# Performance work log

Measured on AMD Instinct MI355X. Metric: run time of the kernel, lower is better.

The kernel has to match this reference:

```python
import jax, jax.numpy as jnp
import numpy as np

NUM_HEADS = 4
B, C, N = 2, 128, 4096
NS = N // 2


def setup_inputs() -> dict:
    key = jax.random.key(0)
    ks = jax.random.split(key, 10)
    # idx_select/idx_drop together form a permutation of [0, N) per batch
    perms = jax.vmap(lambda k: jax.random.permutation(k, N))(jax.random.split(ks[8], B))
    idx_select = perms[:, :NS][:, None, :].astype(jnp.int64)
    idx_drop = perms[:, NS:][:, None, :].astype(jnp.int64)
    return {
        "pcd_up": jax.random.normal(ks[0], (B, C, N), jnp.float32),
        "points_select": jax.random.normal(ks[1], (B, C, NS), jnp.float32),
        "points_drop": jax.random.normal(ks[2], (B, C, NS), jnp.float32),
        "pcd_up_xyz": jax.random.normal(ks[3], (B, 3, N), jnp.float32),
        "Wq": jax.random.normal(ks[4], (C, C), jnp.float32) * 0.05,
        "Wk": jax.random.normal(ks[5], (C, C), jnp.float32) * 0.05,
        "Wv": jax.random.normal(ks[6], (C, C), jnp.float32) * 0.05,
        "Wskip": jax.random.normal(ks[7], (C, C), jnp.float32) * 0.05,
        "idx_select": idx_select,
        "idx_drop": idx_drop,
    }


def _concat_by_idx(a, b, idx_a, idx_b):
    # torch: target.scatter(-1, idx, cat([a,b],-1)) with idx expanded over channels
    src = jnp.concatenate([a, b], axis=-1)                  # [B, C, N]
    idx = jnp.concatenate([idx_a, idx_b], axis=-1)[:, 0, :]  # [B, N]
    return jax.vmap(lambda s, i: jnp.zeros_like(s).at[:, i].set(s))(src, idx)


def reference(pcd_up, points_select, points_drop, pcd_up_xyz, Wq, Wk, Wv, Wskip,
              idx_select, idx_drop):
    x = _concat_by_idx(points_select, points_drop, idx_select, idx_drop)  # [B,C,N]
    b, _, n = x.shape

    def proj_split(W, xx):
        y = jnp.einsum('oc,bcn->bon', W, xx)  # 1x1 Conv1d, no bias
        return y.reshape(b, NUM_HEADS, y.shape[1] // NUM_HEADS, n)  # [B,H,D,N]

    q = proj_split(Wq, x)
    k = proj_split(Wk, x)
    v = proj_split(Wv, x)
    dq = q.shape[2]
    # energy = q^T @ k, scaled by sqrt(q_depth)
    energy = jnp.einsum('bhdn,bhdm->bhnm', q, k) / jnp.sqrt(jnp.asarray(dq, x.dtype))
    attn = jax.nn.softmax(energy, axis=-1)                   # [B,H,N,N]
    out = jnp.einsum('bhnm,bhdm->bhnd', attn, v)             # [B,H,N,Dv]
    out = out.transpose(0, 2, 1, 3).reshape(b, n, -1).transpose(0, 2, 1)  # [B,v_out,N]
    return out + jnp.einsum('oc,bcn->bon', Wskip, pcd_up)
```

## Files before the change

kernel.cpp:

```cpp
#include <hip/hip_runtime.h>
#include <cstdint>

#define B_ 2
#define C_ 128
#define N_ 4096
#define H_ 4
#define D_ 32

typedef unsigned short ushort_t;
typedef __attribute__((ext_vector_type(8))) short bf16x8;
typedef __attribute__((ext_vector_type(4))) float f32x4;
typedef __attribute__((ext_vector_type(4))) unsigned int u32x4;

__device__ __forceinline__ ushort_t f2bf(float f) {
  unsigned int u = __builtin_bit_cast(unsigned int, f);
  u += 0x7fffu + ((u >> 16) & 1u);
  return (ushort_t)(u >> 16);
}

__device__ __forceinline__ void stage16(const ushort_t* g, ushort_t* l) {
  __builtin_amdgcn_global_load_lds(
      (const __attribute__((address_space(1))) unsigned int*)g,
      (__attribute__((address_space(3))) unsigned int*)l, 16, 0, 0);
}

__global__ __launch_bounds__(256) void k_prep(const float* __restrict__ psel,
                                              const float* __restrict__ pdrop,
                                              const int* __restrict__ isel,
                                              const int* __restrict__ idrop,
                                              const float* __restrict__ Wq,
                                              const float* __restrict__ Wk,
                                              const float* __restrict__ Wv,
                                              const float* __restrict__ Wsk,
                                              ushort_t* __restrict__ xT,
                                              ushort_t* __restrict__ Wb) {
  int z = blockIdx.z;
  int t = threadIdx.x;
  if (z == 2) {
    int idx = blockIdx.y * 64 + blockIdx.x;
    int m = idx >> 5, sub = idx & 31;
    const float* src = (m == 0) ? Wq : (m == 1) ? Wk : (m == 2) ? Wv : Wsk;
    float sc = (m == 0) ? 0.25506552f : 1.0f;
    int e = sub * 512 + t * 2;
    float2 v = *(const float2*)(src + e);
    unsigned int u = ((unsigned int)f2bf(v.y * sc) << 16) | (unsigned int)f2bf(v.x * sc);
    ((unsigned int*)Wb)[m * 8192 + (e >> 1)] = u;
    return;
  }
  const float* src = z ? pdrop : psel;
  const int* idx = z ? idrop : isel;
  __shared__ ushort_t tile[128][34];
  int b = blockIdx.y;
  int i0 = blockIdx.x * 32;
  {
    int c = t >> 1, ih = (t & 1) * 16;
    const float4* p = (const float4*)(src + ((size_t)(b * 128 + c) * 2048 + i0 + ih));
#pragma unroll
    for (int g = 0; g < 4; ++g) {
      float4 v = p[g];
      tile[c][ih + g * 4 + 0] = f2bf(v.x);
      tile[c][ih + g * 4 + 1] = f2bf(v.y);
      tile[c][ih + g * 4 + 2] = f2bf(v.z);
      tile[c][ih + g * 4 + 3] = f2bf(v.w);
    }
  }
  __syncthreads();
  {
    int i = t >> 3, c0 = (t & 7) * 16;
    int n = idx[b * 2048 + i0 + i];
    alignas(16) ushort_t outv[16];
#pragma unroll
    for (int j = 0; j < 16; ++j) outv[j] = tile[c0 + j][i];
    uint4* q = (uint4*)(xT + ((size_t)(b * 4096 + n) * 128 + c0));
    q[0] = *(uint4*)outv; q[1] = *(uint4*)(outv + 8);
  }
}

__global__ __launch_bounds__(256) void k_proj(const ushort_t* __restrict__ xT,
                                              const float* __restrict__ pcd,
                                              const ushort_t* __restrict__ Wb,
                                              ushort_t* __restrict__ Kb,
                                              ushort_t* __restrict__ Vt,
                                              float* __restrict__ outp) {
  __shared__ ushort_t ldsT[64][136];
  __shared__ float y[128][66];
  int n0 = blockIdx.x * 64, wt = blockIdx.y, b = blockIdx.z, t = threadIdx.x;
  int wave = t >> 6, lane = t & 63, lr = lane & 15, quad = lane >> 4;
  const ushort_t* W = Wb + (size_t)(wt + 1) * 16384;

  if (wt == 2) {
#pragma unroll
    for (int rep = 0; rep < 4; ++rep) {
      int idx = rep * 256 + t;
      int c = idx >> 3, ng = (idx & 7) * 8;
      const float4* p = (const float4*)(pcd + ((size_t)(b * 128 + c) * 4096 + n0 + ng));
      float4 v0 = p[0], v1 = p[1];
      ldsT[ng + 0][c] = f2bf(v0.x); ldsT[ng + 1][c] = f2bf(v0.y);
      ldsT[ng + 2][c] = f2bf(v0.z); ldsT[ng + 3][c] = f2bf(v0.w);
      ldsT[ng + 4][c] = f2bf(v1.x); ldsT[ng + 5][c] = f2bf(v1.y);
      ldsT[ng + 6][c] = f2bf(v1.z); ldsT[ng + 7][c] = f2bf(v1.w);
    }
    __syncthreads();
  }

  f32x4 acc[2][4];
#pragma unroll
  for (int mt = 0; mt < 2; ++mt)
#pragma unroll
    for (int nt = 0; nt < 4; ++nt) acc[mt][nt] = (f32x4){0.f, 0.f, 0.f, 0.f};
#pragma unroll
  for (int kc = 0; kc < 128; kc += 32) {
    bf16x8 a[2], bb[4];
#pragma unroll
    for (int mt = 0; mt < 2; ++mt)
      a[mt] = *(const bf16x8*)(W + (size_t)(wave * 32 + mt * 16 + lr) * 128 + kc + quad * 8);
    if (wt == 2) {
#pragma unroll
      for (int nt = 0; nt < 4; ++nt)
        bb[nt] = *(const bf16x8*)(&ldsT[nt * 16 + lr][kc + quad * 8]);
    } else {
#pragma unroll
      for (int nt = 0; nt < 4; ++nt)
        bb[nt] = *(const bf16x8*)(xT + ((size_t)(b * 4096 + n0 + nt * 16 + lr)) * 128 + kc + quad * 8);
    }
#pragma unroll
    for (int mt = 0; mt < 2; ++mt)
#pragma unroll
      for (int nt = 0; nt < 4; ++nt)
        acc[mt][nt] = __builtin_amdgcn_mfma_f32_16x16x32_bf16(a[mt], bb[nt], acc[mt][nt], 0, 0, 0);
  }

  if (wt == 2) {
#pragma unroll
    for (int mt = 0; mt < 2; ++mt)
#pragma unroll
      for (int nt = 0; nt < 4; ++nt)
#pragma unroll
        for (int r = 0; r < 4; ++r) {
          int o = wave * 32 + mt * 16 + quad * 4 + r;
          outp[(size_t)(b * 128 + o) * 4096 + n0 + nt * 16 + lr] = acc[mt][nt][r];
        }
    return;
  }

#pragma unroll
  for (int mt = 0; mt < 2; ++mt)
#pragma unroll
    for (int nt = 0; nt < 4; ++nt)
#pragma unroll
      for (int r = 0; r < 4; ++r)
        y[wave * 32 + mt * 16 + quad * 4 + r][nt * 16 + lr] = acc[mt][nt][r];
  __syncthreads();

  if (wt == 0) {
    int n = t >> 2, dq = (t & 3) * 8;
#pragma unroll
    for (int h = 0; h < 4; ++h) {
      alignas(16) ushort_t vals[8];
#pragma unroll
      for (int j = 0; j < 8; ++j) vals[j] = f2bf(y[h * 32 + dq + j][n]);
      *(uint4*)(Kb + (((size_t)(b * 4 + h) * 4096 + n0 + n) * 32 + dq)) = *(uint4*)vals;
    }
  } else {
    int o = t >> 1, half = t & 1;
    int h = o >> 5, d = o & 31;
    alignas(16) ushort_t vals[32];
#pragma unroll
    for (int j = 0; j < 32; ++j) {
      int c = half * 32 + ((j >> 3) * 4 + (j & 3) + ((j & 4) << 2));
      vals[j] = f2bf(y[o][c]);
    }
    uint4* dst = (uint4*)(Vt + ((size_t)(b * 4 + h) * 32 + d) * 4096 + n0 + half * 32);
#pragma unroll
    for (int g = 0; g < 4; ++g) dst[g] = *(uint4*)(vals + g * 8);
  }
}

__global__ __launch_bounds__(256) void k_attn(const ushort_t* __restrict__ xT,
                                              const ushort_t* __restrict__ Wb,
                                              const ushort_t* __restrict__ Kb,
                                              const ushort_t* __restrict__ Vt,
                                              float* __restrict__ outp) {
  __shared__ ushort_t qT[4][32 * 40];
  __shared__ ushort_t kbuf[2][4096];
  __shared__ ushort_t vbuf[2][4096];
  __shared__ float obuf[4][32 * 33];

  int bh = blockIdx.x & 7;
  int q0 = (blockIdx.x >> 3) * 128;
  int b = bh >> 2, h = bh & 3;
  int t = threadIdx.x, wave = t >> 6, lane = t & 63, lr = lane & 15, quad = lane >> 4;
  int qbase = q0 + wave * 32;
  const ushort_t* xb = xT + (size_t)b * N_ * 128;
  const ushort_t* wqp = Wb + (size_t)h * 32 * 128;
  const ushort_t* Kp = Kb + (size_t)bh * N_ * 32;
  const ushort_t* Vp = Vt + (size_t)bh * 32 * N_;

  {
    f32x4 accq[2][2];
#pragma unroll
    for (int mt = 0; mt < 2; ++mt)
#pragma unroll
      for (int nt = 0; nt < 2; ++nt) accq[mt][nt] = (f32x4){0.f, 0.f, 0.f, 0.f};
#pragma unroll
    for (int kc = 0; kc < 128; kc += 32) {
      bf16x8 ax[2], bw[2];
#pragma unroll
      for (int mt = 0; mt < 2; ++mt)
        ax[mt] = *(const bf16x8*)(xb + (size_t)(qbase + mt * 16 + lr) * 128 + kc + quad * 8);
#pragma unroll
      for (int nt = 0; nt < 2; ++nt)
        bw[nt] = *(const bf16x8*)(wqp + (size_t)(nt * 16 + lr) * 128 + kc + quad * 8);
#pragma unroll
      for (int mt = 0; mt < 2; ++mt)
#pragma unroll
        for (int nt = 0; nt < 2; ++nt)
          accq[mt][nt] = __builtin_amdgcn_mfma_f32_16x16x32_bf16(ax[mt], bw[nt], accq[mt][nt], 0, 0, 0);
    }
#pragma unroll
    for (int mt = 0; mt < 2; ++mt)
#pragma unroll
      for (int nt = 0; nt < 2; ++nt)
#pragma unroll
        for (int r = 0; r < 4; ++r)
          qT[wave][(mt * 16 + quad * 4 + r) * 40 + nt * 16 + lr] = f2bf(accq[mt][nt][r]);
  }
  bf16x8 aq0 = *(const bf16x8*)(&qT[wave][lr * 40 + quad * 8]);
  bf16x8 aq1 = *(const bf16x8*)(&qT[wave][(16 + lr) * 40 + quad * 8]);

  f32x4 accO[2][2];
#pragma unroll
  for (int qf = 0; qf < 2; ++qf)
#pragma unroll
    for (int dt = 0; dt < 2; ++dt) accO[qf][dt] = (f32x4){0.f, 0.f, 0.f, 0.f};
  float rsp[2] = {0.f, 0.f};

#define STAGE_CHUNK(kcn, buf)                                                          \
  {                                                                                    \
    ushort_t* kb_ = kbuf[buf];                                                         \
    ushort_t* vb_ = vbuf[buf];                                                         \
    _Pragma("unroll") for (int j = 0; j < 2; ++j) {                                    \
      int s = wave * 2 + j;                                                            \
      stage16(Kp + (size_t)((kcn) + (s & 1) * 64 + lane) * 32 + (s >> 1) * 8,          \
              kb_ + s * 512);                                                          \
      int I = s * 64 + lane;                                                           \
      stage16(Vp + (size_t)(I & 31) * N_ + (kcn) + ((I >> 5) * 8), vb_ + s * 512);     \
    }                                                                                  \
  }

  STAGE_CHUNK(0, 0);
  __syncthreads();

  for (int it = 0; it < 32; ++it) {
    int cur = it & 1;
    if (it + 1 < 32) STAGE_CHUNK((it + 1) * 128, cur ^ 1);
    const ushort_t* kb = kbuf[cur];
    const ushort_t* vb = vbuf[cur];
#pragma unroll
    for (int g = 0; g < 4; ++g) {
      bf16x8 bk0 = *(const bf16x8*)(kb + (quad * 128 + g * 32 + lr) * 8);
      bf16x8 bk1 = *(const bf16x8*)(kb + (quad * 128 + g * 32 + 16 + lr) * 8);
      bf16x8 bv0 = *(const bf16x8*)(vb + ((g * 4 + quad) * 32 + lr) * 8);
      bf16x8 bv1 = *(const bf16x8*)(vb + ((g * 4 + quad) * 32 + 16 + lr) * 8);

      f32x4 z = {0.f, 0.f, 0.f, 0.f};
      f32x4 s0 = __builtin_amdgcn_mfma_f32_16x16x32_bf16(bk0, aq0, z, 0, 0, 0);
      f32x4 s1 = __builtin_amdgcn_mfma_f32_16x16x32_bf16(bk1, aq0, z, 0, 0, 0);
      f32x4 s2 = __builtin_amdgcn_mfma_f32_16x16x32_bf16(bk0, aq1, z, 0, 0, 0);
      f32x4 s3 = __builtin_amdgcn_mfma_f32_16x16x32_bf16(bk1, aq1, z, 0, 0, 0);
      float p0[4], p1[4], p2[4], p3[4];
#pragma unroll
      for (int r = 0; r < 4; ++r) {
        p0[r] = __builtin_amdgcn_exp2f(s0[r]);
        p1[r] = __builtin_amdgcn_exp2f(s1[r]);
        p2[r] = __builtin_amdgcn_exp2f(s2[r]);
        p3[r] = __builtin_amdgcn_exp2f(s3[r]);
        rsp[0] += p0[r] + p1[r];
        rsp[1] += p2[r] + p3[r];
      }
      u32x4 pk0, pk1;
      pk0.x = __builtin_amdgcn_perm(__builtin_bit_cast(unsigned int, p0[1]),
                                    __builtin_bit_cast(unsigned int, p0[0]), 0x07060302u);
      pk0.y = __builtin_amdgcn_perm(__builtin_bit_cast(unsigned int, p0[3]),
                                    __builtin_bit_cast(unsigned int, p0[2]), 0x07060302u);
      pk0.z = __builtin_amdgcn_perm(__builtin_bit_cast(unsigned int, p1[1]),
                                    __builtin_bit_cast(unsigned int, p1[0]), 0x07060302u);
      pk0.w = __builtin_amdgcn_perm(__builtin_bit_cast(unsigned int, p1[3]),
                                    __builtin_bit_cast(unsigned int, p1[2]), 0x07060302u);
      pk1.x = __builtin_amdgcn_perm(__builtin_bit_cast(unsigned int, p2[1]),
                                    __builtin_bit_cast(unsigned int, p2[0]), 0x07060302u);
      pk1.y = __builtin_amdgcn_perm(__builtin_bit_cast(unsigned int, p2[3]),
                                    __builtin_bit_cast(unsigned int, p2[2]), 0x07060302u);
      pk1.z = __builtin_amdgcn_perm(__builtin_bit_cast(unsigned int, p3[1]),
                                    __builtin_bit_cast(unsigned int, p3[0]), 0x07060302u);
      pk1.w = __builtin_amdgcn_perm(__builtin_bit_cast(unsigned int, p3[3]),
                                    __builtin_bit_cast(unsigned int, p3[2]), 0x07060302u);
      bf16x8 ap0 = __builtin_bit_cast(bf16x8, pk0);
      bf16x8 ap1 = __builtin_bit_cast(bf16x8, pk1);
      accO[0][0] = __builtin_amdgcn_mfma_f32_16x16x32_bf16(ap0, bv0, accO[0][0], 0, 0, 0);
      accO[0][1] = __builtin_amdgcn_mfma_f32_16x16x32_bf16(ap0, bv1, accO[0][1], 0, 0, 0);
      accO[1][0] = __builtin_amdgcn_mfma_f32_16x16x32_bf16(ap1, bv0, accO[1][0], 0, 0, 0);
      accO[1][1] = __builtin_amdgcn_mfma_f32_16x16x32_bf16(ap1, bv1, accO[1][1], 0, 0, 0);
    }
    __syncthreads();
  }

  float rinv[2][4];
#pragma unroll
  for (int qf = 0; qf < 2; ++qf) {
    float v = rsp[qf];
    v += __shfl_xor(v, 16);
    v += __shfl_xor(v, 32);
#pragma unroll
    for (int r = 0; r < 4; ++r)
      rinv[qf][r] = 1.0f / __shfl(v, (lane & 48) | (quad * 4 + r), 64);
  }

  float* ob = obuf[wave];
#pragma unroll
  for (int qf = 0; qf < 2; ++qf)
#pragma unroll
    for (int dt = 0; dt < 2; ++dt)
#pragma unroll
      for (int r = 0; r < 4; ++r)
        ob[(dt * 16 + lr) * 33 + qf * 16 + quad * 4 + r] = accO[qf][dt][r] * rinv[qf][r];

  int d = lane >> 1, q16 = (lane & 1) * 16;
  float* po = outp + ((size_t)(b * 128 + h * 32 + d)) * N_ + qbase + q16;
#pragma unroll
  for (int g = 0; g < 4; ++g) {
    float4 r0 = *(float4*)(po + g * 4);
    r0.x += ob[d * 33 + q16 + g * 4 + 0];
    r0.y += ob[d * 33 + q16 + g * 4 + 1];
    r0.z += ob[d * 33 + q16 + g * 4 + 2];
    r0.w += ob[d * 33 + q16 + g * 4 + 3];
    *(float4*)(po + g * 4) = r0;
  }
}

extern "C" void kernel_launch(void* const* d_in, const int* in_sizes, int n_in,
                              void* d_out, int out_size, void* d_ws, size_t ws_size,
                              hipStream_t stream) {
  const float* pcd_up = (const float*)d_in[0];
  const float* psel   = (const float*)d_in[1];
  const float* pdrop  = (const float*)d_in[2];
  const float* Wq  = (const float*)d_in[4];
  const float* Wk  = (const float*)d_in[5];
  const float* Wv  = (const float*)d_in[6];
  const float* Wsk = (const float*)d_in[7];
  const int* isel  = (const int*)d_in[8];
  const int* idrop = (const int*)d_in[9];
  float* out = (float*)d_out;

  ushort_t* xT = (ushort_t*)d_ws;
  ushort_t* Wb = xT + 1048576;
  ushort_t* Kb = Wb + 65536;
  ushort_t* Vt = Kb + 1048576;

  hipLaunchKernelGGL(k_prep, dim3(64, 2, 3), dim3(256), 0, stream,
                     psel, pdrop, isel, idrop, Wq, Wk, Wv, Wsk, xT, Wb);
  hipLaunchKernelGGL(k_proj, dim3(64, 3, 2), dim3(256), 0, stream,
                     xT, pcd_up, Wb, Kb, Vt, out);
  hipLaunchKernelGGL(k_attn, dim3(256), dim3(256), 0, stream, xT, Wb, Kb, Vt, out);
}
```

Before: 136.8 us.

## Split attention key range across two wave groups and compute row sums via MFMA

```diff
diff --git a/kernel.cpp b/kernel.cpp
--- a/kernel.cpp
+++ b/kernel.cpp
@@ -176,71 +176,32 @@
   }
 }
 
-__global__ __launch_bounds__(256) void k_attn(const ushort_t* __restrict__ xT,
+__global__ __launch_bounds__(512) void k_attn(const ushort_t* __restrict__ xT,
                                               const ushort_t* __restrict__ Wb,
                                               const ushort_t* __restrict__ Kb,
                                               const ushort_t* __restrict__ Vt,
                                               float* __restrict__ outp) {
   __shared__ ushort_t qT[4][32 * 40];
-  __shared__ ushort_t kbuf[2][4096];
-  __shared__ ushort_t vbuf[2][4096];
-  __shared__ float obuf[4][32 * 33];
+  __shared__ ushort_t stg[2][2][8192];
 
   int bh = blockIdx.x & 7;
   int q0 = (blockIdx.x >> 3) * 128;
   int b = bh >> 2, h = bh & 3;
   int t = threadIdx.x, wave = t >> 6, lane = t & 63, lr = lane & 15, quad = lane >> 4;
-  int qbase = q0 + wave * 32;
+  int qh = wave & 3, khalf = wave >> 2, lw = qh;
+  int qbase = q0 + qh * 32;
   const ushort_t* xb = xT + (size_t)b * N_ * 128;
   const ushort_t* wqp = Wb + (size_t)h * 32 * 128;
   const ushort_t* Kp = Kb + (size_t)bh * N_ * 32;
   const ushort_t* Vp = Vt + (size_t)bh * 32 * N_;
-
-  {
-    f32x4 accq[2][2];
-#pragma unroll
-    for (int mt = 0; mt < 2; ++mt)
-#pragma unroll
-      for (int nt = 0; nt < 2; ++nt) accq[mt][nt] = (f32x4){0.f, 0.f, 0.f, 0.f};
-#pragma unroll
-    for (int kc = 0; kc < 128; kc += 32) {
-      bf16x8 ax[2], bw[2];
-#pragma unroll
-      for (int mt = 0; mt < 2; ++mt)
-        ax[mt] = *(const bf16x8*)(xb + (size_t)(qbase + mt * 16 + lr) * 128 + kc + quad * 8);
-#pragma unroll
-      for (int nt = 0; nt < 2; ++nt)
-        bw[nt] = *(const bf16x8*)(wqp + (size_t)(nt * 16 + lr) * 128 + kc + quad * 8);
-#pragma unroll
-      for (int mt = 0; mt < 2; ++mt)
-#pragma unroll
-        for (int nt = 0; nt < 2; ++nt)
-          accq[mt][nt] = __builtin_amdgcn_mfma_f32_16x16x32_bf16(ax[mt], bw[nt], accq[mt][nt], 0, 0, 0);
-    }
-#pragma unroll
-    for (int mt = 0; mt < 2; ++mt)
-#pragma unroll
-      for (int nt = 0; nt < 2; ++nt)
-#pragma unroll
-        for (int r = 0; r < 4; ++r)
-          qT[wave][(mt * 16 + quad * 4 + r) * 40 + nt * 16 + lr] = f2bf(accq[mt][nt][r]);
-  }
-  bf16x8 aq0 = *(const bf16x8*)(&qT[wave][lr * 40 + quad * 8]);
-  bf16x8 aq1 = *(const bf16x8*)(&qT[wave][(16 + lr) * 40 + quad * 8]);
-
-  f32x4 accO[2][2];
-#pragma unroll
-  for (int qf = 0; qf < 2; ++qf)
-#pragma unroll
-    for (int dt = 0; dt < 2; ++dt) accO[qf][dt] = (f32x4){0.f, 0.f, 0.f, 0.f};
-  float rsp[2] = {0.f, 0.f};
+  const int ks = khalf * 2048;
 
 #define STAGE_CHUNK(kcn, buf)                                                          \
   {                                                                                    \
-    ushort_t* kb_ = kbuf[buf];                                                         \
-    ushort_t* vb_ = vbuf[buf];                                                         \
+    ushort_t* kb_ = stg[khalf][buf];                                                   \
+    ushort_t* vb_ = kb_ + 4096;                                                        \
     _Pragma("unroll") for (int j = 0; j < 2; ++j) {                                    \
-      int s = wave * 2 + j;                                                            \
+      int s = lw * 2 + j;                                                              \
       stage16(Kp + (size_t)((kcn) + (s & 1) * 64 + lane) * 32 + (s >> 1) * 8,          \
               kb_ + s * 512);                                                          \
       int I = s * 64 + lane;                                                           \
@@ -248,14 +209,60 @@
     }                                                                                  \
   }
 
-  STAGE_CHUNK(0, 0);
+  if (khalf == 0) {
+    f32x4 accq[2][2];
+#pragma unroll
+    for (int mt = 0; mt < 2; ++mt)
+#pragma unroll
+      for (int nt = 0; nt < 2; ++nt) accq[mt][nt] = (f32x4){0.f, 0.f, 0.f, 0.f};
+#pragma unroll
+    for (int kc = 0; kc < 128; kc += 32) {
+      bf16x8 ax[2], bw[2];
+#pragma unroll
+      for (int mt = 0; mt < 2; ++mt)
+        ax[mt] = *(const bf16x8*)(xb + (size_t)(qbase + mt * 16 + lr) * 128 + kc + quad * 8);
+#pragma unroll
+      for (int nt = 0; nt < 2; ++nt)
+        bw[nt] = *(const bf16x8*)(wqp + (size_t)(nt * 16 + lr) * 128 + kc + quad * 8);
+#pragma unroll
+      for (int mt = 0; mt < 2; ++mt)
+#pragma unroll
+        for (int nt = 0; nt < 2; ++nt)
+          accq[mt][nt] = __builtin_amdgcn_mfma_f32_16x16x32_bf16(ax[mt], bw[nt], accq[mt][nt], 0, 0, 0);
+    }
+#pragma unroll
+    for (int mt = 0; mt < 2; ++mt)
+#pragma unroll
+      for (int nt = 0; nt < 2; ++nt)
+#pragma unroll
+        for (int r = 0; r < 4; ++r)
+          qT[qh][(mt * 16 + quad * 4 + r) * 40 + nt * 16 + lr] = f2bf(accq[mt][nt][r]);
+  }
+
+  STAGE_CHUNK(ks, 0);
   __syncthreads();
 
-  for (int it = 0; it < 32; ++it) {
+  bf16x8 aq0 = *(const bf16x8*)(&qT[qh][lr * 40 + quad * 8]);
+  bf16x8 aq1 = *(const bf16x8*)(&qT[qh][(16 + lr) * 40 + quad * 8]);
+
+  bf16x8 vones;
+#pragma unroll
+  for (int j = 0; j < 8; ++j) vones[j] = (short)0x3F80;
+
+  f32x4 accO[2][2];
+  f32x4 accR[2];
+#pragma unroll
+  for (int qf = 0; qf < 2; ++qf) {
+#pragma unroll
+    for (int dt = 0; dt < 2; ++dt) accO[qf][dt] = (f32x4){0.f, 0.f, 0.f, 0.f};
+    accR[qf] = (f32x4){0.f, 0.f, 0.f, 0.f};
+  }
+
+  for (int it = 0; it < 16; ++it) {
     int cur = it & 1;
-    if (it + 1 < 32) STAGE_CHUNK((it + 1) * 128, cur ^ 1);
-    const ushort_t* kb = kbuf[cur];
-    const ushort_t* vb = vbuf[cur];
+    if (it + 1 < 16) STAGE_CHUNK(ks + (it + 1) * 128, cur ^ 1);
+    const ushort_t* kb = stg[khalf][cur];
+    const ushort_t* vb = kb + 4096;
 #pragma unroll
     for (int g = 0; g < 4; ++g) {
       bf16x8 bk0 = *(const bf16x8*)(kb + (quad * 128 + g * 32 + lr) * 8);
@@ -275,8 +282,6 @@
         p1[r] = __builtin_amdgcn_exp2f(s1[r]);
         p2[r] = __builtin_amdgcn_exp2f(s2[r]);
         p3[r] = __builtin_amdgcn_exp2f(s3[r]);
-        rsp[0] += p0[r] + p1[r];
-        rsp[1] += p2[r] + p3[r];
       }
       u32x4 pk0, pk1;
       pk0.x = __builtin_amdgcn_perm(__builtin_bit_cast(unsigned int, p0[1]),
@@ -301,29 +306,55 @@
       accO[0][1] = __builtin_amdgcn_mfma_f32_16x16x32_bf16(ap0, bv1, accO[0][1], 0, 0, 0);
       accO[1][0] = __builtin_amdgcn_mfma_f32_16x16x32_bf16(ap1, bv0, accO[1][0], 0, 0, 0);
       accO[1][1] = __builtin_amdgcn_mfma_f32_16x16x32_bf16(ap1, bv1, accO[1][1], 0, 0, 0);
+      accR[0] = __builtin_amdgcn_mfma_f32_16x16x32_bf16(ap0, vones, accR[0], 0, 0, 0);
+      accR[1] = __builtin_amdgcn_mfma_f32_16x16x32_bf16(ap1, vones, accR[1], 0, 0, 0);
     }
     __syncthreads();
   }
 
-  float rinv[2][4];
+  float* pbuf = (float*)&stg[0][0][0];
+  float* obuf = (float*)((char*)&stg[0][0][0] + 32768);
+
+  if (khalf == 1) {
+    float* pb = pbuf + (qh * 64 + lane) * 24;
+#pragma unroll
+    for (int qf = 0; qf < 2; ++qf) {
+#pragma unroll
+      for (int dt = 0; dt < 2; ++dt)
+#pragma unroll
+        for (int r = 0; r < 4; ++r) pb[qf * 8 + dt * 4 + r] = accO[qf][dt][r];
+#pragma unroll
+      for (int r = 0; r < 4; ++r) pb[16 + qf * 4 + r] = accR[qf][r];
+    }
+  }
+  __syncthreads();
+  if (khalf == 1) return;
+
+  {
+    const float* pb = pbuf + (qh * 64 + lane) * 24;
+#pragma unroll
+    for (int qf = 0; qf < 2; ++qf) {
+#pragma unroll
+      for (int dt = 0; dt < 2; ++dt)
+#pragma unroll
+        for (int r = 0; r < 4; ++r) accO[qf][dt][r] += pb[qf * 8 + dt * 4 + r];
+#pragma unroll
+      for (int r = 0; r < 4; ++r) accR[qf][r] += pb[16 + qf * 4 + r];
+    }
+  }
+
+  float* ob = obuf + qh * 32 * 33;
 #pragma unroll
   for (int qf = 0; qf < 2; ++qf) {
-    float v = rsp[qf];
-    v += __shfl_xor(v, 16);
-    v += __shfl_xor(v, 32);
-#pragma unroll
-    for (int r = 0; r < 4; ++r)
-      rinv[qf][r] = 1.0f / __shfl(v, (lane & 48) | (quad * 4 + r), 64);
-  }
-
-  float* ob = obuf[wave];
-#pragma unroll
-  for (int qf = 0; qf < 2; ++qf)
+    float rinv[4];
+#pragma unroll
+    for (int r = 0; r < 4; ++r) rinv[r] = 1.0f / accR[qf][r];
 #pragma unroll
     for (int dt = 0; dt < 2; ++dt)
 #pragma unroll
       for (int r = 0; r < 4; ++r)
-        ob[(dt * 16 + lr) * 33 + qf * 16 + quad * 4 + r] = accO[qf][dt][r] * rinv[qf][r];
+        ob[(dt * 16 + lr) * 33 + qf * 16 + quad * 4 + r] = accO[qf][dt][r] * rinv[r];
+  }
 
   int d = lane >> 1, q16 = (lane & 1) * 16;
   float* po = outp + ((size_t)(b * 128 + h * 32 + d)) * N_ + qbase + q16;
@@ -361,5 +392,5 @@
                      psel, pdrop, isel, idrop, Wq, Wk, Wv, Wsk, xT, Wb);
   hipLaunchKernelGGL(k_proj, dim3(64, 3, 2), dim3(256), 0, stream,
                      xT, pcd_up, Wb, Kb, Vt, out);
-  hipLaunchKernelGGL(k_attn, dim3(256), dim3(256), 0, stream, xT, Wb, Kb, Vt, out);
-}
+  hipLaunchKernelGGL(k_attn, dim3(256), dim3(512), 0, stream, xT, Wb, Kb, Vt, out);
+}
```

Result: faster. 122.2 us (-10.6%).
